# Kernel tuning notes

Hardware: AMD Instinct MI355X
Metric: run time of the kernel (lower is better)

The kernel has to match this reference:

```python
import jax, jax.numpy as jnp
import numpy as np

N = 100  # n_subcritics; +-1/+-10 neighbor offsets imply a fixed 10x10 grid
OFFSETS = np.array([0, -10, 1, 10, -1])  # neighbor order: (i, i-10, i+1, i+10, i-1)


def _neighbor_gather(x):
    # x: [B, T, N, 7] -> xi: [B, T, N, 35]; out-of-range neighbors contribute zeros
    idx = np.arange(N)[:, None] + OFFSETS[None, :]          # [N, 5]
    mask = (idx >= 0) & (idx < N)
    idx_c = np.clip(idx, 0, N - 1)
    g = x[:, :, idx_c, :] * jnp.asarray(mask, x.dtype)[None, None, :, :, None]
    return g.reshape(x.shape[0], x.shape[1], N, 5 * x.shape[-1])


def _forward(x, lm_W1, lm_b1, lm_W2, lm_b2, lm_W3, lm_b3,
             gru_Wih, gru_Whh, gru_bih, gru_bhh,
             sc_W1, sc_b1, sc_W2, sc_b2, sc_W3, sc_b3):
    xi = _neighbor_gather(x)                                 # [B, T, N, 35]
    # LocalizedModule (per-node MLP) on the last timestep
    xl = xi[:, -1]                                           # [B, N, 35]
    h = jax.nn.relu(jnp.einsum('bnf,nfh->bnh', xl, lm_W1) + lm_b1)
    h = jax.nn.relu(jnp.einsum('bnf,nfh->bnh', h, lm_W2) + lm_b2)
    f = jnp.einsum('bnf,nfo->bno', h, lm_W3) + lm_b3         # [B, N, 1]
    # SubCritic: per-node GRU (PyTorch gate order r, z, n) over time, then MLP on final hidden
    def step(hc, xt):
        gi = jnp.einsum('bnf,ngf->bng', xt, gru_Wih) + gru_bih   # [B, N, 48]
        gh = jnp.einsum('bnh,ngh->bng', hc, gru_Whh) + gru_bhh
        ir, iz, i_n = jnp.split(gi, 3, axis=-1)
        hr, hz, h_n = jnp.split(gh, 3, axis=-1)
        r = jax.nn.sigmoid(ir + hr)
        z = jax.nn.sigmoid(iz + hz)
        n = jnp.tanh(i_n + r * h_n)
        return (1.0 - z) * n + z * hc, None
    h0 = jnp.zeros((x.shape[0], N, gru_Whh.shape[-1]), x.dtype)
    hT, _ = jax.lax.scan(step, h0, jnp.moveaxis(xi, 1, 0))   # final hidden [B, N, 16]
    g = jax.nn.relu(jnp.einsum('bnf,nfh->bnh', hT, sc_W1) + sc_b1)
    g = jax.nn.relu(jnp.einsum('bnf,nfh->bnh', g, sc_W2) + sc_b2)
    q = jnp.einsum('bnf,nfo->bno', g, sc_W3) + sc_b3         # [B, N, 1]
    # torch.cat over node-major lists of [B,1] then sum(dim=1) -> [N*B]
    return jnp.transpose(f[..., 0] + q[..., 0]).reshape(-1)


def setup_inputs():
    key = jax.random.key(0)
    ks = jax.random.split(key, 18)
    B, T, S, G = 128, 256, 7, 16
    def w(k, shape, scale=0.05):
        return jax.random.normal(k, shape, dtype=jnp.float32) * scale
    return {
        'x': jax.random.normal(ks[0], (B, T, N, S), dtype=jnp.float32),
        'lm_W1': w(ks[1], (N, 35, 512)), 'lm_b1': w(ks[2], (N, 512)),
        'lm_W2': w(ks[3], (N, 512, 256)), 'lm_b2': w(ks[4], (N, 256)),
        'lm_W3': w(ks[5], (N, 256, 1)), 'lm_b3': w(ks[6], (N, 1)),
        'gru_Wih': w(ks[7], (N, 3 * G, 35)), 'gru_Whh': w(ks[8], (N, 3 * G, G)),
        'gru_bih': w(ks[9], (N, 3 * G)), 'gru_bhh': w(ks[10], (N, 3 * G)),
        'sc_W1': w(ks[11], (N, G, G)), 'sc_b1': w(ks[12], (N, G)),
        'sc_W2': w(ks[13], (N, G, G)), 'sc_b2': w(ks[14], (N, G)),
        'sc_W3': w(ks[15], (N, G, 1)), 'sc_b3': w(ks[16], (N, 1)),
    }


def reference(x, lm_W1, lm_b1, lm_W2, lm_b2, lm_W3, lm_b3,
              gru_Wih, gru_Whh, gru_bih, gru_bhh,
              sc_W1, sc_b1, sc_W2, sc_b2, sc_W3, sc_b3):
    return _forward(x, lm_W1, lm_b1, lm_W2, lm_b2, lm_W3, lm_b3,
                    gru_Wih, gru_Whh, gru_bih, gru_bhh,
                    sc_W1, sc_b1, sc_W2, sc_b2, sc_W3, sc_b3)
```

## Files before the change

kernel.cpp:

```cpp
#include <hip/hip_runtime.h>
#include <cstddef>

#define NN 100
#define TT 256
#define BB 128
#define SS 7
#define FF 35
#define GG 16

typedef __attribute__((ext_vector_type(4))) float f32x4;
typedef __attribute__((ext_vector_type(8))) short short8;

__constant__ int c_off[5] = {0, -10, 1, 10, -1};

__device__ __forceinline__ float sigmoidf_(float v) {
  return 1.0f / (1.0f + __expf(-v));
}
__device__ __forceinline__ float tanhf_(float v) {
  return 1.0f - 2.0f / (__expf(2.0f * v) + 1.0f);
}
__device__ __forceinline__ unsigned bf1(float a) {
  unsigned u = __float_as_uint(a);
  return (u + 0x7FFFu + ((u >> 16) & 1u)) >> 16;
}
__device__ __forceinline__ unsigned bfp(float lo, float hi) {
  return bf1(lo) | (bf1(hi) << 16);
}

__global__ void __launch_bounds__(512)
k_lm1(const float* __restrict__ x, const float* __restrict__ W1,
      const float* __restrict__ b1, float* __restrict__ H1) {
  const int bc = blockIdx.x;
  const int n  = blockIdx.y;
  const int b0 = bc * 32;
  const int tid = threadIdx.x;
  __shared__ __align__(16) float xl[32][36];
  for (int idx = tid; idx < 32 * FF; idx += 512) {
    const int bb = idx / FF, f = idx % FF;
    const int m = n + c_off[f / SS];
    const int s = f % SS;
    float v = 0.0f;
    if (m >= 0 && m < NN)
      v = x[(((size_t)(b0 + bb) * TT + (TT - 1)) * NN + m) * SS + s];
    xl[bb][f] = v;
  }
  __syncthreads();
  const int h = tid;
  float w[FF];
  const float* wp = W1 + (size_t)n * FF * 512 + h;
#pragma unroll
  for (int f = 0; f < FF; ++f) w[f] = wp[(size_t)f * 512];
  const float bias = b1[n * 512 + h];
  for (int bb = 0; bb < 32; ++bb) {
    const float4* xr = (const float4*)(&xl[bb][0]);
    float acc = bias;
#pragma unroll
    for (int q = 0; q < 8; ++q) {
      const float4 v = xr[q];
      acc += w[4*q+0] * v.x + w[4*q+1] * v.y + w[4*q+2] * v.z + w[4*q+3] * v.w;
    }
    {
      const float4 v = xr[8];
      acc += w[32] * v.x + w[33] * v.y + w[34] * v.z;
    }
    H1[((size_t)(b0 + bb) * NN + n) * 512 + h] = fmaxf(acc, 0.0f);
  }
}

__global__ void __launch_bounds__(256)
k_lm2(const float* __restrict__ H1, const float* __restrict__ W2,
      const float* __restrict__ b2, float* __restrict__ H2) {
  const int n  = blockIdx.x;
  const int bh = blockIdx.y >> 2;
  const int ch = blockIdx.y & 3;
  const int tid = threadIdx.x;
  const int tc = tid & 15;
  const int tb = tid >> 4;
  __shared__ __align__(16) float A[32][68];
  __shared__ __align__(16) float Bt[32][68];
  float acc[4][4];
#pragma unroll
  for (int i = 0; i < 4; ++i)
#pragma unroll
    for (int j = 0; j < 4; ++j) acc[i][j] = 0.0f;

  for (int k0 = 0; k0 < 512; k0 += 32) {
    __syncthreads();
    for (int l = tid; l < 512; l += 256) {
      const int bi = l >> 3, kq = l & 7;
      const float4 v = *(const float4*)(&H1[((size_t)(bh*64 + bi) * NN + n) * 512 + k0 + kq*4]);
      A[kq*4+0][bi] = v.x; A[kq*4+1][bi] = v.y; A[kq*4+2][bi] = v.z; A[kq*4+3][bi] = v.w;
    }
    for (int l = tid; l < 512; l += 256) {
      const int kk = l >> 4, c4 = l & 15;
      const float4 v = *(const float4*)(&W2[((size_t)n * 512 + (k0 + kk)) * 256 + ch*64 + c4*4]);
      *(float4*)(&Bt[kk][c4*4]) = v;
    }
    __syncthreads();
#pragma unroll 8
    for (int k = 0; k < 32; ++k) {
      const float4 a4 = *(const float4*)(&A[k][tb*4]);
      const float4 b4 = *(const float4*)(&Bt[k][tc*4]);
      const float av[4] = {a4.x, a4.y, a4.z, a4.w};
      const float bv[4] = {b4.x, b4.y, b4.z, b4.w};
#pragma unroll
      for (int i = 0; i < 4; ++i)
#pragma unroll
        for (int j = 0; j < 4; ++j) acc[i][j] += av[i] * bv[j];
    }
  }
#pragma unroll
  for (int i = 0; i < 4; ++i) {
    const int b = bh*64 + tb*4 + i;
    const int c0 = ch*64 + tc*4;
    const float* bp = b2 + n*256 + c0;
    float4 o;
    o.x = fmaxf(acc[i][0] + bp[0], 0.0f);
    o.y = fmaxf(acc[i][1] + bp[1], 0.0f);
    o.z = fmaxf(acc[i][2] + bp[2], 0.0f);
    o.w = fmaxf(acc[i][3] + bp[3], 0.0f);
    *(float4*)(&H2[((size_t)b * NN + n) * 256 + c0]) = o;
  }
}

__global__ void __launch_bounds__(256)
k_lm3(const float* __restrict__ H2, const float* __restrict__ W3,
      const float* __restrict__ b3, float* __restrict__ out) {
  const int w = threadIdx.x >> 6;
  const int lane = threadIdx.x & 63;
  const int p = blockIdx.x * 4 + w;
  const int b = p / NN, n = p % NN;
  const float4 hv = *(const float4*)(&H2[((size_t)b * NN + n) * 256 + lane*4]);
  const float4 wv = *(const float4*)(&W3[n * 256 + lane*4]);
  float dot = hv.x*wv.x + hv.y*wv.y + hv.z*wv.z + hv.w*wv.w;
#pragma unroll
  for (int off = 32; off > 0; off >>= 1) dot += __shfl_down(dot, off);
  if (lane == 0) out[n * BB + b] = dot + b3[n];
}

#define DOT16(acc, u0, u1, u2, u3, h0, h1, h2, h3)             \
  acc += u0.x*h0.x + u0.y*h0.y + u0.z*h0.z + u0.w*h0.w;        \
  acc += u1.x*h1.x + u1.y*h1.y + u1.z*h1.z + u1.w*h1.w;        \
  acc += u2.x*h2.x + u2.y*h2.y + u2.z*h2.z + u2.w*h2.w;        \
  acc += u3.x*h3.x + u3.y*h3.y + u3.z*h3.z + u3.w*h3.w;

__global__ void __launch_bounds__(64, 3)
k_gru(const float* __restrict__ x,
      const float* __restrict__ Wih, const float* __restrict__ Whh,
      const float* __restrict__ bih, const float* __restrict__ bhh,
      const float* __restrict__ sW1, const float* __restrict__ sb1,
      const float* __restrict__ sW2, const float* __restrict__ sb2,
      const float* __restrict__ sW3, const float* __restrict__ sb3,
      float* __restrict__ out) {
  const int l  = threadIdx.x;
  const int g  = l & 15;
  const int b  = l >> 4;
  const int kg = b;
  const int ab = (l & 15) >> 2;
  const int atoff = l & 3;
  const int bc = blockIdx.x;
  const int n  = blockIdx.y;
  const int bga = bc*4 + ab;
  const int bgp = bc*4 + b;

  __shared__ float hlds[4][16];

  const float* wh = Whh + ((size_t)n*48 + g)*GG;
  const float4 ur0 = *(const float4*)(wh+0),  ur1 = *(const float4*)(wh+4),
               ur2 = *(const float4*)(wh+8),  ur3 = *(const float4*)(wh+12);
  const float4 uz0 = *(const float4*)(wh+256),  uz1 = *(const float4*)(wh+260),
               uz2 = *(const float4*)(wh+264),  uz3 = *(const float4*)(wh+268);
  const float4 un0 = *(const float4*)(wh+512),  un1 = *(const float4*)(wh+516),
               un2 = *(const float4*)(wh+520),  un3 = *(const float4*)(wh+524);
  const float bir = bih[n*48 + g], biz = bih[n*48 + 16 + g], bin_ = bih[n*48 + 32 + g];
  const float bhr = bhh[n*48 + g], bhz = bhh[n*48 + 16 + g], bhn = bhh[n*48 + 32 + g];

  short8 bw[3], bw2[3];
#pragma unroll
  for (int c = 0; c < 3; ++c) {
    const float* wp = Wih + ((size_t)n*48 + c*16 + g)*FF;
    float t0_[8], t1_[8];
#pragma unroll
    for (int j = 0; j < 8; ++j) t0_[j] = wp[kg*8 + j];
#pragma unroll
    for (int j = 0; j < 8; ++j) {
      const int k2 = 32 + kg*8 + j;
      t1_[j] = (k2 < FF) ? wp[k2] : 0.0f;
    }
    union { short8 s; unsigned u[4]; } U, V;
#pragma unroll
    for (int jj = 0; jj < 4; ++jj) { U.u[jj] = bfp(t0_[2*jj], t0_[2*jj+1]);
                                     V.u[jj] = bfp(t1_[2*jj], t1_[2*jj+1]); }
    bw[c] = U.s; bw2[c] = V.s;
  }

  int adelta[8]; unsigned amask = 0;
#pragma unroll
  for (int j = 0; j < 8; ++j) {
    const int f  = kg*8 + j;
    const int fi = (f * 586) >> 12;
    const int s  = f - fi*7;
    const int mo = (fi == 0) ? 0 : (fi == 1) ? -10 : (fi == 2) ? 1 : (fi == 3) ? 10 : -1;
    adelta[j] = mo*SS + s;
    const int m = n + mo;
    if (m >= 0 && m < NN) amask |= (1u << j);
  }
  const bool v2 = (kg == 0) && (n >= 1);

  float xv[8], xv2[3];
  {
    const float* xq = x + ((size_t)bga*TT + atoff)*(NN*SS) + n*SS;
#pragma unroll
    for (int j = 0; j < 8; ++j) xv[j] = ((amask >> j) & 1u) ? xq[adelta[j]] : 0.0f;
#pragma unroll
    for (int j = 0; j < 3; ++j) xv2[j] = v2 ? xq[-3 + j] : 0.0f;
  }

  hlds[b][g] = 0.0f;
  float hown = 0.0f;

  const f32x4 z4 = {0.0f, 0.0f, 0.0f, 0.0f};

  for (int rd = 0; rd < TT/4; ++rd) {
    union { short8 s; unsigned u[4]; } A1, A2;
#pragma unroll
    for (int jj = 0; jj < 4; ++jj) A1.u[jj] = bfp(xv[2*jj], xv[2*jj+1]);
    A2.u[0] = bfp(xv2[0], xv2[1]); A2.u[1] = bfp(xv2[2], 0.0f); A2.u[2] = 0; A2.u[3] = 0;
    const short8 af1 = A1.s, af2 = A2.s;

    if (rd < TT/4 - 1) {
      const float* xq = x + ((size_t)bga*TT + (rd*4 + 4 + atoff))*(NN*SS) + n*SS;
#pragma unroll
      for (int j = 0; j < 8; ++j) xv[j] = ((amask >> j) & 1u) ? xq[adelta[j]] : 0.0f;
#pragma unroll
      for (int j = 0; j < 3; ++j) xv2[j] = v2 ? xq[-3 + j] : 0.0f;
    }

    f32x4 c0 = __builtin_amdgcn_mfma_f32_16x16x32_bf16(af1, bw[0], z4, 0, 0, 0);
    c0 = __builtin_amdgcn_mfma_f32_16x16x32_bf16(af2, bw2[0], c0, 0, 0, 0);
    f32x4 c1 = __builtin_amdgcn_mfma_f32_16x16x32_bf16(af1, bw[1], z4, 0, 0, 0);
    c1 = __builtin_amdgcn_mfma_f32_16x16x32_bf16(af2, bw2[1], c1, 0, 0, 0);
    f32x4 c2 = __builtin_amdgcn_mfma_f32_16x16x32_bf16(af1, bw[2], z4, 0, 0, 0);
    c2 = __builtin_amdgcn_mfma_f32_16x16x32_bf16(af2, bw2[2], c2, 0, 0, 0);

#pragma unroll
    for (int toff = 0; toff < 4; ++toff) {
      const float ir  = c0[toff] + bir;
      const float iz  = c1[toff] + biz;
      const float in_ = c2[toff] + bin_;
      const float4* hp = (const float4*)(&hlds[b][0]);
      const float4 h0 = hp[0], h1 = hp[1], h2 = hp[2], h3 = hp[3];
      float hr = bhr, hz = bhz, hn = bhn;
      DOT16(hr, ur0, ur1, ur2, ur3, h0, h1, h2, h3)
      DOT16(hz, uz0, uz1, uz2, uz3, h0, h1, h2, h3)
      DOT16(hn, un0, un1, un2, un3, h0, h1, h2, h3)
      const float r   = sigmoidf_(ir + hr);
      const float z   = sigmoidf_(iz + hz);
      const float nn2 = tanhf_(in_ + r * hn);
      const float hnew = nn2 + z * (hown - nn2);
      hlds[b][g] = hnew;
      hown = hnew;
    }
  }

  {
    const float4* hp = (const float4*)(&hlds[b][0]);
    const float4 h0 = hp[0], h1 = hp[1], h2 = hp[2], h3 = hp[3];
    const float* w1 = sW1 + n*GG*GG + g;
    float a1 = sb1[n*GG + g];
    a1 += h0.x*w1[0*GG] + h0.y*w1[1*GG] + h0.z*w1[2*GG] + h0.w*w1[3*GG];
    a1 += h1.x*w1[4*GG] + h1.y*w1[5*GG] + h1.z*w1[6*GG] + h1.w*w1[7*GG];
    a1 += h2.x*w1[8*GG] + h2.y*w1[9*GG] + h2.z*w1[10*GG] + h2.w*w1[11*GG];
    a1 += h3.x*w1[12*GG] + h3.y*w1[13*GG] + h3.z*w1[14*GG] + h3.w*w1[15*GG];
    a1 = fmaxf(a1, 0.0f);
    hlds[b][g] = a1;
  }
  {
    const float4* hp = (const float4*)(&hlds[b][0]);
    const float4 h0 = hp[0], h1 = hp[1], h2 = hp[2], h3 = hp[3];
    const float* w2 = sW2 + n*GG*GG + g;
    float a2 = sb2[n*GG + g];
    a2 += h0.x*w2[0*GG] + h0.y*w2[1*GG] + h0.z*w2[2*GG] + h0.w*w2[3*GG];
    a2 += h1.x*w2[4*GG] + h1.y*w2[5*GG] + h1.z*w2[6*GG] + h1.w*w2[7*GG];
    a2 += h2.x*w2[8*GG] + h2.y*w2[9*GG] + h2.z*w2[10*GG] + h2.w*w2[11*GG];
    a2 += h3.x*w2[12*GG] + h3.y*w2[13*GG] + h3.z*w2[14*GG] + h3.w*w2[15*GG];
    a2 = fmaxf(a2, 0.0f);
    float p = a2 * sW3[n*GG + g];
    p += __shfl_xor(p, 1);
    p += __shfl_xor(p, 2);
    p += __shfl_xor(p, 4);
    p += __shfl_xor(p, 8);
    if (g == 0) out[n * BB + bgp] += p + sb3[n];
  }
}

extern "C" void kernel_launch(void* const* d_in, const int* in_sizes, int n_in,
                              void* d_out, int out_size, void* d_ws, size_t ws_size,
                              hipStream_t stream) {
  const float* x     = (const float*)d_in[0];
  const float* lm_W1 = (const float*)d_in[1];
  const float* lm_b1 = (const float*)d_in[2];
  const float* lm_W2 = (const float*)d_in[3];
  const float* lm_b2 = (const float*)d_in[4];
  const float* lm_W3 = (const float*)d_in[5];
  const float* lm_b3 = (const float*)d_in[6];
  const float* gWih  = (const float*)d_in[7];
  const float* gWhh  = (const float*)d_in[8];
  const float* gbih  = (const float*)d_in[9];
  const float* gbhh  = (const float*)d_in[10];
  const float* sW1   = (const float*)d_in[11];
  const float* sb1   = (const float*)d_in[12];
  const float* sW2   = (const float*)d_in[13];
  const float* sb2   = (const float*)d_in[14];
  const float* sW3   = (const float*)d_in[15];
  const float* sb3   = (const float*)d_in[16];
  float* out = (float*)d_out;

  float* H1 = (float*)d_ws;
  float* H2 = (float*)((char*)d_ws + (size_t)BB * NN * 512 * 4);

  k_lm1<<<dim3(4, NN), 512, 0, stream>>>(x, lm_W1, lm_b1, H1);
  k_lm2<<<dim3(NN, 8), 256, 0, stream>>>(H1, lm_W2, lm_b2, H2);
  k_lm3<<<dim3(3200), 256, 0, stream>>>(H2, lm_W3, lm_b3, out);
  k_gru<<<dim3(32, NN), 64, 0, stream>>>(x, gWih, gWhh, gbih, gbhh,
                                         sW1, sb1, sW2, sb2, sW3, sb3, out);
}
```

Baseline: 539.8 us.

## Use bf16 MFMA for LM layer-2 GEMM and cheapen GRU math

Replaces the shared-memory FP32 SGEMM in the second localized-MLP layer with per-wave bf16 MFMA 16x16x32 tiles that load operands straight from global memory, launching 3200 blocks. The GRU gates switch division to hardware reciprocal, bf16 packing switches from round-to-nearest to truncation, and the recurrent dot products are split into a tree reduction to shorten dependency chains. These trade accuracy (bf16 truncation, approximate rcp) for fewer FP32 ops and a shorter serial critical path in the recurrence. The new GEMM drops LDS reuse, so W2 column loads are strided scalar reads.

```diff
diff --git a/kernel.cpp b/kernel.cpp
--- a/kernel.cpp
+++ b/kernel.cpp
@@ -14,10 +14,10 @@
 __constant__ int c_off[5] = {0, -10, 1, 10, -1};
 
 __device__ __forceinline__ float sigmoidf_(float v) {
-  return 1.0f / (1.0f + __expf(-v));
+  return __builtin_amdgcn_rcpf(1.0f + __expf(-v));
 }
 __device__ __forceinline__ float tanhf_(float v) {
-  return 1.0f - 2.0f / (__expf(2.0f * v) + 1.0f);
+  return 1.0f - 2.0f * __builtin_amdgcn_rcpf(__expf(2.0f * v) + 1.0f);
 }
 __device__ __forceinline__ unsigned bf1(float a) {
   unsigned u = __float_as_uint(a);
@@ -25,6 +25,9 @@
 }
 __device__ __forceinline__ unsigned bfp(float lo, float hi) {
   return bf1(lo) | (bf1(hi) << 16);
+}
+__device__ __forceinline__ unsigned pkt(float lo, float hi) {
+  return (__float_as_uint(lo) >> 16) | (__float_as_uint(hi) & 0xFFFF0000u);
 }
 
 __global__ void __launch_bounds__(512)
@@ -69,57 +72,43 @@
 
 __global__ void __launch_bounds__(256)
 k_lm2(const float* __restrict__ H1, const float* __restrict__ W2,
-      const float* __restrict__ b2, float* __restrict__ H2) {
-  const int n  = blockIdx.x;
-  const int bh = blockIdx.y >> 2;
-  const int ch = blockIdx.y & 3;
-  const int tid = threadIdx.x;
-  const int tc = tid & 15;
-  const int tb = tid >> 4;
-  __shared__ __align__(16) float A[32][68];
-  __shared__ __align__(16) float Bt[32][68];
-  float acc[4][4];
-#pragma unroll
-  for (int i = 0; i < 4; ++i)
-#pragma unroll
-    for (int j = 0; j < 4; ++j) acc[i][j] = 0.0f;
-
+      const float* __restrict__ bias2, float* __restrict__ H2) {
+  const int w  = threadIdx.x >> 6;
+  const int l  = threadIdx.x & 63;
+  const int n  = blockIdx.x >> 5;
+  const int tg = blockIdx.x & 31;
+  const int tau = tg * 4 + w;
+  const int rt = tau >> 4;
+  const int ct = tau & 15;
+  const int lr = l & 15;
+  const int kg = l >> 4;
+
+  const int arow = rt * 16 + lr;
+  const int col  = ct * 16 + lr;
+
+  const float* Ab = H1 + ((size_t)arow * NN + n) * 512 + kg * 8;
+  const float* Bb = W2 + (size_t)n * 512 * 256 + (size_t)(kg * 8) * 256 + col;
+
+  f32x4 acc = {0.0f, 0.0f, 0.0f, 0.0f};
+#pragma unroll 2
   for (int k0 = 0; k0 < 512; k0 += 32) {
-    __syncthreads();
-    for (int l = tid; l < 512; l += 256) {
-      const int bi = l >> 3, kq = l & 7;
-      const float4 v = *(const float4*)(&H1[((size_t)(bh*64 + bi) * NN + n) * 512 + k0 + kq*4]);
-      A[kq*4+0][bi] = v.x; A[kq*4+1][bi] = v.y; A[kq*4+2][bi] = v.z; A[kq*4+3][bi] = v.w;
-    }
-    for (int l = tid; l < 512; l += 256) {
-      const int kk = l >> 4, c4 = l & 15;
-      const float4 v = *(const float4*)(&W2[((size_t)n * 512 + (k0 + kk)) * 256 + ch*64 + c4*4]);
-      *(float4*)(&Bt[kk][c4*4]) = v;
-    }
-    __syncthreads();
-#pragma unroll 8
-    for (int k = 0; k < 32; ++k) {
-      const float4 a4 = *(const float4*)(&A[k][tb*4]);
-      const float4 b4 = *(const float4*)(&Bt[k][tc*4]);
-      const float av[4] = {a4.x, a4.y, a4.z, a4.w};
-      const float bv[4] = {b4.x, b4.y, b4.z, b4.w};
-#pragma unroll
-      for (int i = 0; i < 4; ++i)
-#pragma unroll
-        for (int j = 0; j < 4; ++j) acc[i][j] += av[i] * bv[j];
-    }
-  }
-#pragma unroll
-  for (int i = 0; i < 4; ++i) {
-    const int b = bh*64 + tb*4 + i;
-    const int c0 = ch*64 + tc*4;
-    const float* bp = b2 + n*256 + c0;
-    float4 o;
-    o.x = fmaxf(acc[i][0] + bp[0], 0.0f);
-    o.y = fmaxf(acc[i][1] + bp[1], 0.0f);
-    o.z = fmaxf(acc[i][2] + bp[2], 0.0f);
-    o.w = fmaxf(acc[i][3] + bp[3], 0.0f);
-    *(float4*)(&H2[((size_t)b * NN + n) * 256 + c0]) = o;
+    const float4 a0 = *(const float4*)(Ab + k0);
+    const float4 a1 = *(const float4*)(Ab + k0 + 4);
+    const float* bp = Bb + (size_t)k0 * 256;
+    const float w0 = bp[0],    w1 = bp[256],  w2 = bp[512],  w3 = bp[768];
+    const float w4 = bp[1024], w5 = bp[1280], w6 = bp[1536], w7 = bp[1792];
+    union { short8 s; unsigned u[4]; } A, B;
+    A.u[0] = pkt(a0.x, a0.y); A.u[1] = pkt(a0.z, a0.w);
+    A.u[2] = pkt(a1.x, a1.y); A.u[3] = pkt(a1.z, a1.w);
+    B.u[0] = pkt(w0, w1); B.u[1] = pkt(w2, w3);
+    B.u[2] = pkt(w4, w5); B.u[3] = pkt(w6, w7);
+    acc = __builtin_amdgcn_mfma_f32_16x16x32_bf16(A.s, B.s, acc, 0, 0, 0);
+  }
+  const float bv = bias2[n * 256 + col];
+#pragma unroll
+  for (int r = 0; r < 4; ++r) {
+    const int grow = rt * 16 + kg * 4 + r;
+    H2[((size_t)grow * NN + n) * 256 + col] = fmaxf(acc[r] + bv, 0.0f);
   }
 }
 
@@ -138,11 +127,16 @@
   if (lane == 0) out[n * BB + b] = dot + b3[n];
 }
 
-#define DOT16(acc, u0, u1, u2, u3, h0, h1, h2, h3)             \
-  acc += u0.x*h0.x + u0.y*h0.y + u0.z*h0.z + u0.w*h0.w;        \
-  acc += u1.x*h1.x + u1.y*h1.y + u1.z*h1.z + u1.w*h1.w;        \
-  acc += u2.x*h2.x + u2.y*h2.y + u2.z*h2.z + u2.w*h2.w;        \
-  acc += u3.x*h3.x + u3.y*h3.y + u3.z*h3.z + u3.w*h3.w;
+__device__ __forceinline__ float dot16s(const float4 u0, const float4 u1,
+                                        const float4 u2, const float4 u3,
+                                        const float4 h0, const float4 h1,
+                                        const float4 h2, const float4 h3) {
+  const float p0 = u0.x*h0.x + u0.y*h0.y + u0.z*h0.z + u0.w*h0.w;
+  const float p1 = u1.x*h1.x + u1.y*h1.y + u1.z*h1.z + u1.w*h1.w;
+  const float p2 = u2.x*h2.x + u2.y*h2.y + u2.z*h2.z + u2.w*h2.w;
+  const float p3 = u3.x*h3.x + u3.y*h3.y + u3.z*h3.z + u3.w*h3.w;
+  return (p0 + p1) + (p2 + p3);
+}
 
 __global__ void __launch_bounds__(64, 3)
 k_gru(const float* __restrict__ x,
@@ -224,8 +218,8 @@
   for (int rd = 0; rd < TT/4; ++rd) {
     union { short8 s; unsigned u[4]; } A1, A2;
 #pragma unroll
-    for (int jj = 0; jj < 4; ++jj) A1.u[jj] = bfp(xv[2*jj], xv[2*jj+1]);
-    A2.u[0] = bfp(xv2[0], xv2[1]); A2.u[1] = bfp(xv2[2], 0.0f); A2.u[2] = 0; A2.u[3] = 0;
+    for (int jj = 0; jj < 4; ++jj) A1.u[jj] = pkt(xv[2*jj], xv[2*jj+1]);
+    A2.u[0] = pkt(xv2[0], xv2[1]); A2.u[1] = pkt(xv2[2], 0.0f); A2.u[2] = 0; A2.u[3] = 0;
     const short8 af1 = A1.s, af2 = A2.s;
 
     if (rd < TT/4 - 1) {
@@ -250,10 +244,9 @@
       const float in_ = c2[toff] + bin_;
       const float4* hp = (const float4*)(&hlds[b][0]);
       const float4 h0 = hp[0], h1 = hp[1], h2 = hp[2], h3 = hp[3];
-      float hr = bhr, hz = bhz, hn = bhn;
-      DOT16(hr, ur0, ur1, ur2, ur3, h0, h1, h2, h3)
-      DOT16(hz, uz0, uz1, uz2, uz3, h0, h1, h2, h3)
-      DOT16(hn, un0, un1, un2, un3, h0, h1, h2, h3)
+      const float hr = bhr + dot16s(ur0, ur1, ur2, ur3, h0, h1, h2, h3);
+      const float hz = bhz + dot16s(uz0, uz1, uz2, uz3, h0, h1, h2, h3);
+      const float hn = bhn + dot16s(un0, un1, un2, un3, h0, h1, h2, h3);
       const float r   = sigmoidf_(ir + hr);
       const float z   = sigmoidf_(iz + hz);
       const float nn2 = tanhf_(in_ + r * hn);
@@ -320,7 +313,7 @@
   float* H2 = (float*)((char*)d_ws + (size_t)BB * NN * 512 * 4);
 
   k_lm1<<<dim3(4, NN), 512, 0, stream>>>(x, lm_W1, lm_b1, H1);
-  k_lm2<<<dim3(NN, 8), 256, 0, stream>>>(H1, lm_W2, lm_b2, H2);
+  k_lm2<<<dim3(3200), 256, 0, stream>>>(H1, lm_W2, lm_b2, H2);
   k_lm3<<<dim3(3200), 256, 0, stream>>>(H2, lm_W3, lm_b3, out);
   k_gru<<<dim3(32, NN), 64, 0, stream>>>(x, gWih, gWhh, gbih, gbhh,
                                          sW1, sb1, sW2, sb2, sW3, sb3, out);
```

New measurement: 542.4 us. Within noise of the previous version (+0.5%).
